# Kernel tuning notes

Measured on AMD Instinct MI355X. Metric: run time of the kernel, lower is better.

## Reference

```python
import jax, jax.numpy as jnp
import numpy as np

N0, N1, N2 = 200000, 100000, 50000
E0, E1 = 1600000, 800000
D_IN, H, C, K = 256, 256, 7, 40  # in_feats, n_hidden, center_num, n_classes


def setup_inputs() -> dict:
    key = jax.random.key(0)
    ks = jax.random.split(key, 11)
    s = 0.05
    inputs = jax.random.normal(ks[0], (N0, D_IN), jnp.float32)
    edge_src0 = jax.random.randint(ks[1], (E0,), 0, N0, jnp.int32)
    edge_dst0 = jax.random.randint(ks[2], (E0,), 0, N1, jnp.int32)
    edge_src1 = jax.random.randint(ks[3], (E1,), 0, N1, jnp.int32)
    edge_dst1 = jax.random.randint(ks[4], (E1,), 0, N2, jnp.int32)
    W_self0 = jax.random.normal(ks[5], (H, D_IN), jnp.float32) * s
    W_neigh0 = jax.random.normal(ks[6], (H, D_IN), jnp.float32) * s
    b0 = jnp.zeros((H,), jnp.float32)
    W_self1 = jax.random.normal(ks[7], (H, H), jnp.float32) * s
    W_neigh1 = jax.random.normal(ks[8], (H, H), jnp.float32) * s
    b1 = jnp.zeros((H,), jnp.float32)
    W_prompt = jax.random.normal(ks[9], (C, 2 * H), jnp.float32) * s
    W_pp = jax.random.normal(ks[10], (C, K, 2 * H), jnp.float32) * s
    return dict(inputs=inputs, W_self0=W_self0, W_neigh0=W_neigh0, b0=b0,
                W_self1=W_self1, W_neigh1=W_neigh1, b1=b1,
                W_prompt=W_prompt, W_pp=W_pp,
                edge_src0=edge_src0, edge_dst0=edge_dst0,
                edge_src1=edge_src1, edge_dst1=edge_dst1)


def _sage_conv(h_src, h_dst, esrc, edst, n_dst, W_self, W_neigh, b):
    # DGL SAGEConv('mean'): fc_self(h_dst) + fc_neigh(mean_{u in N(v)} h_src[u]) + bias
    msg = h_src[esrc]                                            # [E, d]
    summ = jax.ops.segment_sum(msg, edst, num_segments=n_dst)    # [n_dst, d]
    deg = jax.ops.segment_sum(jnp.ones((esrc.shape[0],), msg.dtype), edst,
                              num_segments=n_dst)                # [n_dst]
    mean = summ / jnp.maximum(deg, 1.0)[:, None]
    return h_dst @ W_self.T + mean @ W_neigh.T + b


def _forward(inputs, W_self0, W_neigh0, b0, W_self1, W_neigh1, b1,
             W_prompt, W_pp, edge_src0, edge_dst0, edge_src1, edge_dst1):
    h = inputs  # dropout=0.0 (eval): identity
    # layer 0: N0 src -> N1 dst
    h_dst = h[:N1]
    h = _sage_conv(h, h_dst, edge_src0, edge_dst0, N1, W_self0, W_neigh0, b0)
    h = jax.nn.relu(h)
    # layer 1: N1 src -> N2 dst
    h_dst = h[:N2]
    h = _sage_conv(h, h_dst, edge_src1, edge_dst1, N2, W_self1, W_neigh1, b1)
    h = jax.nn.relu(h)
    neighbor = jax.nn.relu(h_dst)
    hcat = jnp.concatenate([h, neighbor], axis=1)                # [N2, 2H]
    scores = hcat @ W_prompt.T                                   # [N2, C]
    index = jnp.argmax(scores, axis=1)                           # [N2]
    # per-cluster expert Linear, top-1 dispatch/combine
    all_out = jnp.einsum('nd,ckd->nck', hcat, W_pp)              # [N2, C, K]
    out = jnp.take_along_axis(all_out, index[:, None, None], axis=1)[:, 0, :]
    return out


def reference(inputs, W_self0, W_neigh0, b0, W_self1, W_neigh1, b1,
              W_prompt, W_pp, edge_src0, edge_dst0, edge_src1, edge_dst1):
    return _forward(inputs, W_self0, W_neigh0, b0, W_self1, W_neigh1, b1,
                    W_prompt, W_pp, edge_src0, edge_dst0, edge_src1, edge_dst1)
```

## Files before the change

### kernel.cpp

```cpp
#include <hip/hip_runtime.h>
#include <stdint.h>

typedef unsigned short u16;
typedef unsigned int   u32;
typedef float f32x4  __attribute__((ext_vector_type(4)));
typedef _Float16 f16x4 __attribute__((ext_vector_type(4)));
typedef _Float16 f16x8 __attribute__((ext_vector_type(8)));

#define NN0 200000
#define NN1 100000
#define NN2 50000
#define EE0 1600000
#define EE1 800000
#define DD  256
#define CC  7
#define KK  40

#define LVL2_U16 4096
#define IMG_U16  8192

static __device__ __forceinline__ void split2(float x, _Float16& t0, _Float16& t1) {
    t0 = (_Float16)x;
    t1 = (_Float16)(x - (float)t0);
}

static __device__ __forceinline__ f16x8 pack8(const _Float16* h) {
    f16x8 v;
#pragma unroll
    for (int i = 0; i < 8; ++i) v[i] = h[i];
    return v;
}

static __device__ __forceinline__ void async16(const void* g, void* l) {
    __builtin_amdgcn_global_load_lds(
        (const __attribute__((address_space(1))) void*)g,
        (__attribute__((address_space(3))) void*)l, 16, 0, 0);
}

__global__ void hist_kernel(const int* __restrict__ dst, int* __restrict__ cnt, int n) {
    int i = blockIdx.x * blockDim.x + threadIdx.x;
    if (i < n) atomicAdd(&cnt[dst[i]], 1);
}

__global__ void scan_block_kernel(const int* __restrict__ in, int* __restrict__ out,
                                  int* __restrict__ partials, int n) {
    __shared__ int sd[256];
    int t = threadIdx.x;
    int base = blockIdx.x * 1024 + t * 4;
    int v0 = (base + 0 < n) ? in[base + 0] : 0;
    int v1 = (base + 1 < n) ? in[base + 1] : 0;
    int v2 = (base + 2 < n) ? in[base + 2] : 0;
    int v3 = (base + 3 < n) ? in[base + 3] : 0;
    int p0 = v0, p1 = p0 + v1, p2 = p1 + v2, p3 = p2 + v3;
    sd[t] = p3;
    __syncthreads();
    for (int off = 1; off < 256; off <<= 1) {
        int x = (t >= off) ? sd[t - off] : 0;
        __syncthreads();
        sd[t] += x;
        __syncthreads();
    }
    int excl = sd[t] - p3;
    if (base + 0 < n) out[base + 0] = excl + p0;
    if (base + 1 < n) out[base + 1] = excl + p1;
    if (base + 2 < n) out[base + 2] = excl + p2;
    if (base + 3 < n) out[base + 3] = excl + p3;
    if (t == 255) partials[blockIdx.x] = sd[255];
}

__global__ void scan_partials_kernel(int* __restrict__ partials, int nb) {
    __shared__ int sd[256];
    int t = threadIdx.x;
    int v = (t < nb) ? partials[t] : 0;
    sd[t] = v;
    __syncthreads();
    for (int off = 1; off < 256; off <<= 1) {
        int x = (t >= off) ? sd[t - off] : 0;
        __syncthreads();
        sd[t] += x;
        __syncthreads();
    }
    if (t < nb) partials[t] = sd[t];
}

__global__ void scan_add_kernel(int* __restrict__ out, const int* __restrict__ partials, int n) {
    int b = blockIdx.x;
    if (b == 0) return;
    int add = partials[b - 1];
    int base = b * 1024 + threadIdx.x * 4;
    if (base + 0 < n) out[base + 0] += add;
    if (base + 1 < n) out[base + 1] += add;
    if (base + 2 < n) out[base + 2] += add;
    if (base + 3 < n) out[base + 3] += add;
}

__global__ void fill_kernel(const int* __restrict__ esrc, const int* __restrict__ edst,
                            const int* __restrict__ rp, int* __restrict__ cur,
                            int* __restrict__ ss, int n) {
    int i = blockIdx.x * blockDim.x + threadIdx.x;
    if (i < n) {
        int d = edst[i];
        int p = rp[d] + atomicAdd(&cur[d], 1);
        ss[p] = esrc[i];
    }
}

__global__ void to_fp16(const float* __restrict__ in, _Float16* __restrict__ outp, long n) {
    long i = ((long)blockIdx.x * blockDim.x + threadIdx.x) * 8;
    if (i >= n) return;
    f32x4 a = *reinterpret_cast<const f32x4*>(in + i);
    f32x4 b = *reinterpret_cast<const f32x4*>(in + i + 4);
    f16x8 h;
    h[0] = (_Float16)a[0]; h[1] = (_Float16)a[1]; h[2] = (_Float16)a[2]; h[3] = (_Float16)a[3];
    h[4] = (_Float16)b[0]; h[5] = (_Float16)b[1]; h[6] = (_Float16)b[2]; h[7] = (_Float16)b[3];
    *reinterpret_cast<f16x8*>(outp + i) = h;
}

__global__ void gather_mean_fp16(const _Float16* __restrict__ Xh, const int* __restrict__ rp,
                                 const int* __restrict__ ss, float* __restrict__ mean, int ndst) {
    int wave = threadIdx.x >> 6, lane = threadIdx.x & 63;
    int d = blockIdx.x * 4 + wave;
    if (d >= ndst) return;
    int beg = rp[d], end = rp[d + 1];
    int lo4 = lane * 4;
    f32x4 a0 = (f32x4)(0.f), a1 = (f32x4)(0.f), a2 = (f32x4)(0.f), a3 = (f32x4)(0.f);
    int j = beg;
    for (; j + 8 <= end; j += 8) {
        int s0 = ss[j + 0], s1 = ss[j + 1], s2 = ss[j + 2], s3 = ss[j + 3];
        int s4 = ss[j + 4], s5 = ss[j + 5], s6 = ss[j + 6], s7 = ss[j + 7];
        f16x4 h0 = *reinterpret_cast<const f16x4*>(Xh + (size_t)s0 * DD + lo4);
        f16x4 h1 = *reinterpret_cast<const f16x4*>(Xh + (size_t)s1 * DD + lo4);
        f16x4 h2 = *reinterpret_cast<const f16x4*>(Xh + (size_t)s2 * DD + lo4);
        f16x4 h3 = *reinterpret_cast<const f16x4*>(Xh + (size_t)s3 * DD + lo4);
        f16x4 h4 = *reinterpret_cast<const f16x4*>(Xh + (size_t)s4 * DD + lo4);
        f16x4 h5 = *reinterpret_cast<const f16x4*>(Xh + (size_t)s5 * DD + lo4);
        f16x4 h6 = *reinterpret_cast<const f16x4*>(Xh + (size_t)s6 * DD + lo4);
        f16x4 h7 = *reinterpret_cast<const f16x4*>(Xh + (size_t)s7 * DD + lo4);
        a0 += __builtin_convertvector(h0, f32x4);
        a1 += __builtin_convertvector(h1, f32x4);
        a2 += __builtin_convertvector(h2, f32x4);
        a3 += __builtin_convertvector(h3, f32x4);
        a0 += __builtin_convertvector(h4, f32x4);
        a1 += __builtin_convertvector(h5, f32x4);
        a2 += __builtin_convertvector(h6, f32x4);
        a3 += __builtin_convertvector(h7, f32x4);
    }
    for (; j + 4 <= end; j += 4) {
        int s0 = ss[j + 0], s1 = ss[j + 1], s2 = ss[j + 2], s3 = ss[j + 3];
        f16x4 h0 = *reinterpret_cast<const f16x4*>(Xh + (size_t)s0 * DD + lo4);
        f16x4 h1 = *reinterpret_cast<const f16x4*>(Xh + (size_t)s1 * DD + lo4);
        f16x4 h2 = *reinterpret_cast<const f16x4*>(Xh + (size_t)s2 * DD + lo4);
        f16x4 h3 = *reinterpret_cast<const f16x4*>(Xh + (size_t)s3 * DD + lo4);
        a0 += __builtin_convertvector(h0, f32x4);
        a1 += __builtin_convertvector(h1, f32x4);
        a2 += __builtin_convertvector(h2, f32x4);
        a3 += __builtin_convertvector(h3, f32x4);
    }
    for (; j < end; ++j) {
        int s = ss[j];
        f16x4 h0 = *reinterpret_cast<const f16x4*>(Xh + (size_t)s * DD + lo4);
        a0 += __builtin_convertvector(h0, f32x4);
    }
    f32x4 s = (a0 + a1) + (a2 + a3);
    int dg = end - beg;
    float inv = 1.0f / (float)(dg > 0 ? dg : 1);
    s *= inv;
    *reinterpret_cast<f32x4*>(mean + (size_t)d * DD + lo4) = s;
}

__global__ void build_wimg(const float* __restrict__ Wa0, const float* __restrict__ Wb0,
                           const float* __restrict__ Wa1, const float* __restrict__ Wb1,
                           u16* __restrict__ img) {
    int blk = blockIdx.x;
    int layer = blk >> 5;
    int ntile = (blk >> 4) & 1;
    int chunk = blk & 15;
    const float* Wa = layer ? Wa1 : Wa0;
    const float* Wb = layer ? Wb1 : Wb0;
    int t = threadIdx.x;
    int row = t >> 1, half = t & 1;
    int n = ntile * 128 + row;
    int kg = chunk * 32 + half * 16;
    const float* W = (kg < 256) ? Wa : Wb;
    int kk = kg & 255;
    const float* src = W + (size_t)n * 256 + kk;
    float x[16];
#pragma unroll
    for (int j = 0; j < 16; j += 4) {
        float4 v = *reinterpret_cast<const float4*>(src + j);
        x[j] = v.x; x[j + 1] = v.y; x[j + 2] = v.z; x[j + 3] = v.w;
    }
    _Float16 h0[16], h1[16];
#pragma unroll
    for (int j = 0; j < 16; ++j) split2(x[j], h0[j], h1[j]);
    int rs = (row >> 1) & 3;
    int q0 = (half * 2 + 0) ^ rs;
    int q1 = (half * 2 + 1) ^ rs;
    u16* base = img + (size_t)blk * IMG_U16 + row * 32;
    *reinterpret_cast<f16x8*>(base + q0 * 8)            = pack8(h0);
    *reinterpret_cast<f16x8*>(base + q1 * 8)            = pack8(h0 + 8);
    *reinterpret_cast<f16x8*>(base + LVL2_U16 + q0 * 8) = pack8(h1);
    *reinterpret_cast<f16x8*>(base + LVL2_U16 + q1 * 8) = pack8(h1 + 8);
}

__global__ __launch_bounds__(256, 3) void gemm_f16(const float* __restrict__ X0,
                                                   const float* __restrict__ X1,
                                                   const u16* __restrict__ imgL,
                                                   const float* __restrict__ bias,
                                                   float* __restrict__ out,
                                                   _Float16* __restrict__ outh, int M) {
    __shared__ __align__(16) u16 Asl[2 * LVL2_U16];
    __shared__ __align__(16) u16 Bsl[2 * LVL2_U16];
    int t = threadIdx.x;
    int wave = t >> 6, lane = t & 63;
    int m0 = blockIdx.x * 128;
    int ntile = blockIdx.y;
    int wy = wave >> 1, wx = wave & 1;

    f32x4 acc[4][4];
#pragma unroll
    for (int i = 0; i < 4; ++i)
#pragma unroll
        for (int j = 0; j < 4; ++j) acc[i][j] = (f32x4)(0.f);

    int arow_l = t >> 1;
    int akh = t & 1;
    int arow = m0 + arow_l; if (arow >= M) arow = M - 1;

    int fr = lane & 15;
    int q  = lane >> 4;
    int frm = wy * 64 + fr;
    int frn = wx * 64 + fr;

    const u16* imgT = imgL + (size_t)ntile * 16 * IMG_U16;

    for (int c = 0; c < 16; ++c) {
        const char* src = (const char*)(imgT + (size_t)c * IMG_U16);
#pragma unroll
        for (int i = 0; i < 4; ++i) {
            int seg = wave * 4 + i;
            async16(src + seg * 1024 + lane * 16, (char*)Bsl + seg * 1024 + lane * 16);
        }
        {
            const float* Xs = (c < 8) ? X0 : X1;
            int kc = (c & 7) * 32;
            const float* p = Xs + (size_t)arow * 256 + kc + akh * 16;
            float x[16];
#pragma unroll
            for (int j = 0; j < 16; j += 4) {
                float4 v = *reinterpret_cast<const float4*>(p + j);
                x[j] = v.x; x[j + 1] = v.y; x[j + 2] = v.z; x[j + 3] = v.w;
            }
            _Float16 h0[16], h1[16];
#pragma unroll
            for (int j = 0; j < 16; ++j) split2(x[j], h0[j], h1[j]);
            int rs = (arow_l >> 1) & 3;
            int q0 = (akh * 2 + 0) ^ rs;
            int q1 = (akh * 2 + 1) ^ rs;
            u16* d = Asl + arow_l * 32;
            *reinterpret_cast<f16x8*>(d + q0 * 8)            = pack8(h0);
            *reinterpret_cast<f16x8*>(d + q1 * 8)            = pack8(h0 + 8);
            *reinterpret_cast<f16x8*>(d + LVL2_U16 + q0 * 8) = pack8(h1);
            *reinterpret_cast<f16x8*>(d + LVL2_U16 + q1 * 8) = pack8(h1 + 8);
        }
        __syncthreads();
        f16x8 bf[4][2];
#pragma unroll
        for (int ns = 0; ns < 4; ++ns) {
            int r = frn + ns * 16;
            int off = r * 32 + ((q ^ ((r >> 1) & 3))) * 8;
            bf[ns][0] = *reinterpret_cast<const f16x8*>(Bsl + off);
            bf[ns][1] = *reinterpret_cast<const f16x8*>(Bsl + LVL2_U16 + off);
        }
#pragma unroll
        for (int ms = 0; ms < 4; ++ms) {
            int r = frm + ms * 16;
            int off = r * 32 + ((q ^ ((r >> 1) & 3))) * 8;
            f16x8 af0 = *reinterpret_cast<const f16x8*>(Asl + off);
            f16x8 af1 = *reinterpret_cast<const f16x8*>(Asl + LVL2_U16 + off);
#pragma unroll
            for (int ns = 0; ns < 4; ++ns) {
                f32x4 a = acc[ms][ns];
                a = __builtin_amdgcn_mfma_f32_16x16x32_f16(af0, bf[ns][0], a, 0, 0, 0);
                a = __builtin_amdgcn_mfma_f32_16x16x32_f16(af0, bf[ns][1], a, 0, 0, 0);
                a = __builtin_amdgcn_mfma_f32_16x16x32_f16(af1, bf[ns][0], a, 0, 0, 0);
                acc[ms][ns] = a;
            }
        }
        __syncthreads();
    }
#pragma unroll
    for (int ms = 0; ms < 4; ++ms) {
        int rbase = m0 + wy * 64 + ms * 16 + (lane >> 4) * 4;
#pragma unroll
        for (int ns = 0; ns < 4; ++ns) {
            int col = ntile * 128 + wx * 64 + ns * 16 + (lane & 15);
            float bcol = bias[col];
#pragma unroll
            for (int r = 0; r < 4; ++r) {
                int row = rbase + r;
                if (row < M) {
                    float v = fmaxf(acc[ms][ns][r] + bcol, 0.f);
                    out[(size_t)row * DD + col] = v;
                    if (outh) outh[(size_t)row * DD + col] = (_Float16)v;
                }
            }
        }
    }
}

__global__ void final_kernel(const float* __restrict__ h2, const float* __restrict__ h1,
                             const float* __restrict__ Wp, const float* __restrict__ Wpp,
                             float* __restrict__ out) {
    int wave = threadIdx.x >> 6, lane = threadIdx.x & 63;
    int nd = blockIdx.x * 4 + wave;
    if (nd >= NN2) return;
    int d0 = lane * 8;
    const float* src = (d0 < 256) ? (h2 + (size_t)nd * DD + d0)
                                  : (h1 + (size_t)nd * DD + (d0 - 256));
    float4 v0 = *reinterpret_cast<const float4*>(src);
    float4 v1 = *reinterpret_cast<const float4*>(src + 4);
    float x[8] = {v0.x, v0.y, v0.z, v0.w, v1.x, v1.y, v1.z, v1.w};

    float best = -3.0e38f; int bc = 0;
#pragma unroll
    for (int c = 0; c < CC; ++c) {
        const float* w = Wp + (size_t)c * 512 + d0;
        float4 w0 = *reinterpret_cast<const float4*>(w);
        float4 w1 = *reinterpret_cast<const float4*>(w + 4);
        float p = x[0] * w0.x + x[1] * w0.y + x[2] * w0.z + x[3] * w0.w
                + x[4] * w1.x + x[5] * w1.y + x[6] * w1.z + x[7] * w1.w;
        p += __shfl_xor(p, 32); p += __shfl_xor(p, 16); p += __shfl_xor(p, 8);
        p += __shfl_xor(p, 4);  p += __shfl_xor(p, 2);  p += __shfl_xor(p, 1);
        if (p > best) { best = p; bc = c; }
    }
    for (int k = 0; k < KK; ++k) {
        const float* w = Wpp + ((size_t)bc * KK + k) * 512 + d0;
        float4 w0 = *reinterpret_cast<const float4*>(w);
        float4 w1 = *reinterpret_cast<const float4*>(w + 4);
        float p = x[0] * w0.x + x[1] * w0.y + x[2] * w0.z + x[3] * w0.w
                + x[4] * w1.x + x[5] * w1.y + x[6] * w1.z + x[7] * w1.w;
        p += __shfl_xor(p, 32); p += __shfl_xor(p, 16); p += __shfl_xor(p, 8);
        p += __shfl_xor(p, 4);  p += __shfl_xor(p, 2);  p += __shfl_xor(p, 1);
        if (lane == 0) out[(size_t)nd * KK + k] = p;
    }
}

extern "C" void kernel_launch(void* const* d_in, const int* in_sizes, int n_in,
                              void* d_out, int out_size, void* d_ws, size_t ws_size,
                              hipStream_t stream) {
    const float* inputs  = (const float*)d_in[0];
    const float* Wself0  = (const float*)d_in[1];
    const float* Wneigh0 = (const float*)d_in[2];
    const float* b0      = (const float*)d_in[3];
    const float* Wself1  = (const float*)d_in[4];
    const float* Wneigh1 = (const float*)d_in[5];
    const float* b1      = (const float*)d_in[6];
    const float* Wp      = (const float*)d_in[7];
    const float* Wpp     = (const float*)d_in[8];
    const int* es0 = (const int*)d_in[9];
    const int* ed0 = (const int*)d_in[10];
    const int* es1 = (const int*)d_in[11];
    const int* ed1 = (const int*)d_in[12];

    char* ws = (char*)d_ws;
    size_t off = 0;
    auto alloc = [&](size_t bytes) -> void* {
        void* p = (void*)(ws + off);
        off += (bytes + 255) & ~(size_t)255;
        return p;
    };
    int* cnt0 = (int*)alloc((size_t)NN1 * 4);
    int* cnt1 = (int*)alloc((size_t)NN2 * 4);
    int* cur0 = (int*)alloc((size_t)NN1 * 4);
    int* cur1 = (int*)alloc((size_t)NN2 * 4);
    int* rp0  = (int*)alloc((size_t)(NN1 + 1) * 4);
    int* rp1  = (int*)alloc((size_t)(NN2 + 1) * 4);
    int* part0 = (int*)alloc(1024);
    int* part1 = (int*)alloc(1024);
    size_t zero_bytes = off;
    int*   ss0   = (int*)alloc((size_t)EE0 * 4);
    int*   ss1   = (int*)alloc((size_t)EE1 * 4);
    u16*   wimg  = (u16*)alloc((size_t)64 * IMG_U16 * 2);
    _Float16* xh = (_Float16*)alloc((size_t)NN0 * DD * 2);
    float*    h1 = (float*)xh;
    _Float16* h1h  = (_Float16*)alloc((size_t)NN1 * DD * 2);
    float* mean0 = (float*)alloc((size_t)NN1 * DD * 4);
    float* mean1 = mean0;
    float* h2    = mean0 + (size_t)NN2 * DD;

    hipMemsetAsync(d_ws, 0, zero_bytes, stream);

    hist_kernel<<<(EE0 + 255) / 256, 256, 0, stream>>>(ed0, cnt0, EE0);
    hist_kernel<<<(EE1 + 255) / 256, 256, 0, stream>>>(ed1, cnt1, EE1);
    int nb0 = (NN1 + 1023) / 1024, nb1 = (NN2 + 1023) / 1024;
    scan_block_kernel<<<nb0, 256, 0, stream>>>(cnt0, rp0 + 1, part0, NN1);
    scan_partials_kernel<<<1, 256, 0, stream>>>(part0, nb0);
    scan_add_kernel<<<nb0, 256, 0, stream>>>(rp0 + 1, part0, NN1);
    scan_block_kernel<<<nb1, 256, 0, stream>>>(cnt1, rp1 + 1, part1, NN2);
    scan_partials_kernel<<<1, 256, 0, stream>>>(part1, nb1);
    scan_add_kernel<<<nb1, 256, 0, stream>>>(rp1 + 1, part1, NN2);
    fill_kernel<<<(EE0 + 255) / 256, 256, 0, stream>>>(es0, ed0, rp0, cur0, ss0, EE0);
    fill_kernel<<<(EE1 + 255) / 256, 256, 0, stream>>>(es1, ed1, rp1, cur1, ss1, EE1);

    build_wimg<<<64, 256, 0, stream>>>(Wself0, Wneigh0, Wself1, Wneigh1, wimg);

    long nx = (long)NN0 * DD;
    to_fp16<<<(int)(nx / 8 / 256), 256, 0, stream>>>(inputs, xh, nx);

    gather_mean_fp16<<<(NN1 + 3) / 4, 256, 0, stream>>>(xh, rp0, ss0, mean0, NN1);
    dim3 g0((NN1 + 127) / 128, 2);
    gemm_f16<<<g0, 256, 0, stream>>>(inputs, mean0, wimg, b0, h1, h1h, NN1);

    gather_mean_fp16<<<(NN2 + 3) / 4, 256, 0, stream>>>(h1h, rp1, ss1, mean1, NN2);
    dim3 g1((NN2 + 127) / 128, 2);
    gemm_f16<<<g1, 256, 0, stream>>>(h1, mean1, wimg + (size_t)32 * IMG_U16, b1, h2, nullptr, NN2);

    final_kernel<<<(NN2 + 3) / 4, 256, 0, stream>>>(h2, h1, Wp, Wpp, (float*)d_out);
}
```

Measured before the change: 1.114 ms.

## Split final head into scoring, per-cluster bucketing, and grouped expert projection

The fused final kernel is replaced by four kernels. One computes argmax cluster scores with 16 lanes per node, the next two build counts and a node list grouped by cluster, and the last computes the expert projection over nodes sorted by cluster. Sorting nodes by cluster lets neighbouring waves share the same expert weights in cache, and narrower 16-lane reductions cut the number of shuffles. The cost is three extra launches and an extra pass that re-reads the node features.

```diff
diff --git a/kernel.cpp b/kernel.cpp
--- a/kernel.cpp
+++ b/kernel.cpp
@@ -309,40 +309,99 @@
     }
 }
 
-__global__ void final_kernel(const float* __restrict__ h2, const float* __restrict__ h1,
-                             const float* __restrict__ Wp, const float* __restrict__ Wpp,
-                             float* __restrict__ out) {
-    int wave = threadIdx.x >> 6, lane = threadIdx.x & 63;
-    int nd = blockIdx.x * 4 + wave;
-    if (nd >= NN2) return;
-    int d0 = lane * 8;
-    const float* src = (d0 < 256) ? (h2 + (size_t)nd * DD + d0)
-                                  : (h1 + (size_t)nd * DD + (d0 - 256));
-    float4 v0 = *reinterpret_cast<const float4*>(src);
-    float4 v1 = *reinterpret_cast<const float4*>(src + 4);
-    float x[8] = {v0.x, v0.y, v0.z, v0.w, v1.x, v1.y, v1.z, v1.w};
-
+__global__ void score_kernel(const float* __restrict__ h2, const float* __restrict__ h1,
+                             const float* __restrict__ Wp, int* __restrict__ bcout,
+                             int* __restrict__ gcnt) {
+    __shared__ int lcnt[CC];
+    int t = threadIdx.x;
+    if (t < CC) lcnt[t] = 0;
+    __syncthreads();
+    int wave = t >> 6, lane = t & 63;
+    int ns = lane >> 4, g = lane & 15;
+    int n = (blockIdx.x * 4 + wave) * 4 + ns;
+    int d0 = g * 32;
+    const float* src = (d0 < 256) ? (h2 + (size_t)n * DD + d0)
+                                  : (h1 + (size_t)n * DD + (d0 - 256));
+    f32x4 x[8];
+#pragma unroll
+    for (int j = 0; j < 8; ++j) x[j] = *reinterpret_cast<const f32x4*>(src + j * 4);
     float best = -3.0e38f; int bc = 0;
 #pragma unroll
     for (int c = 0; c < CC; ++c) {
         const float* w = Wp + (size_t)c * 512 + d0;
-        float4 w0 = *reinterpret_cast<const float4*>(w);
-        float4 w1 = *reinterpret_cast<const float4*>(w + 4);
-        float p = x[0] * w0.x + x[1] * w0.y + x[2] * w0.z + x[3] * w0.w
-                + x[4] * w1.x + x[5] * w1.y + x[6] * w1.z + x[7] * w1.w;
-        p += __shfl_xor(p, 32); p += __shfl_xor(p, 16); p += __shfl_xor(p, 8);
-        p += __shfl_xor(p, 4);  p += __shfl_xor(p, 2);  p += __shfl_xor(p, 1);
+        f32x4 a = (f32x4)(0.f);
+#pragma unroll
+        for (int j = 0; j < 8; ++j)
+            a += x[j] * *reinterpret_cast<const f32x4*>(w + j * 4);
+        float p = (a[0] + a[1]) + (a[2] + a[3]);
+        p += __shfl_xor(p, 1, 16);
+        p += __shfl_xor(p, 2, 16);
+        p += __shfl_xor(p, 4, 16);
+        p += __shfl_xor(p, 8, 16);
         if (p > best) { best = p; bc = c; }
     }
+    if (g == 0) {
+        bcout[n] = bc;
+        atomicAdd(&lcnt[bc], 1);
+    }
+    __syncthreads();
+    if (t < CC) atomicAdd(&gcnt[t], lcnt[t]);
+}
+
+__global__ void scan7_kernel(const int* __restrict__ gcnt, int* __restrict__ cbase,
+                             int* __restrict__ cur7) {
+    if (threadIdx.x == 0 && blockIdx.x == 0) {
+        int s = 0;
+        for (int c = 0; c < CC; ++c) { cbase[c] = s; s += gcnt[c]; cur7[c] = 0; }
+        cbase[CC] = s;
+    }
+}
+
+__global__ void fillc_kernel(const int* __restrict__ bc, const int* __restrict__ cbase,
+                             int* __restrict__ cur7, int* __restrict__ nlist) {
+    __shared__ int lcnt[CC];
+    __shared__ int lbase[CC];
+    int t = threadIdx.x;
+    int n = blockIdx.x * 256 + t;
+    if (t < CC) lcnt[t] = 0;
+    __syncthreads();
+    int c = 0, myofs = 0;
+    bool act = n < NN2;
+    if (act) { c = bc[n]; myofs = atomicAdd(&lcnt[c], 1); }
+    __syncthreads();
+    if (t < CC) lbase[t] = lcnt[t] ? atomicAdd(&cur7[t], lcnt[t]) : 0;
+    __syncthreads();
+    if (act) nlist[cbase[c] + lbase[c] + myofs] = n;
+}
+
+__global__ void proj_kernel(const float* __restrict__ h2, const float* __restrict__ h1,
+                            const float* __restrict__ Wpp, const int* __restrict__ nlist,
+                            const int* __restrict__ bcin, float* __restrict__ out) {
+    int t = threadIdx.x;
+    int wave = t >> 6, lane = t & 63;
+    int ns = lane >> 4, g = lane & 15;
+    int i = (blockIdx.x * 4 + wave) * 4 + ns;
+    int n = nlist[i];
+    int c = bcin[n];
+    int d0 = g * 32;
+    const float* src = (d0 < 256) ? (h2 + (size_t)n * DD + d0)
+                                  : (h1 + (size_t)n * DD + (d0 - 256));
+    f32x4 x[8];
+#pragma unroll
+    for (int j = 0; j < 8; ++j) x[j] = *reinterpret_cast<const f32x4*>(src + j * 4);
+    const float* wb = Wpp + (size_t)c * KK * 512 + d0;
     for (int k = 0; k < KK; ++k) {
-        const float* w = Wpp + ((size_t)bc * KK + k) * 512 + d0;
-        float4 w0 = *reinterpret_cast<const float4*>(w);
-        float4 w1 = *reinterpret_cast<const float4*>(w + 4);
-        float p = x[0] * w0.x + x[1] * w0.y + x[2] * w0.z + x[3] * w0.w
-                + x[4] * w1.x + x[5] * w1.y + x[6] * w1.z + x[7] * w1.w;
-        p += __shfl_xor(p, 32); p += __shfl_xor(p, 16); p += __shfl_xor(p, 8);
-        p += __shfl_xor(p, 4);  p += __shfl_xor(p, 2);  p += __shfl_xor(p, 1);
-        if (lane == 0) out[(size_t)nd * KK + k] = p;
+        const float* w = wb + (size_t)k * 512;
+        f32x4 a = (f32x4)(0.f);
+#pragma unroll
+        for (int j = 0; j < 8; ++j)
+            a += x[j] * *reinterpret_cast<const f32x4*>(w + j * 4);
+        float p = (a[0] + a[1]) + (a[2] + a[3]);
+        p += __shfl_xor(p, 1, 16);
+        p += __shfl_xor(p, 2, 16);
+        p += __shfl_xor(p, 4, 16);
+        p += __shfl_xor(p, 8, 16);
+        if (g == (k & 15)) out[(size_t)n * KK + k] = p;
     }
 }
 
@@ -378,9 +437,14 @@
     int* rp1  = (int*)alloc((size_t)(NN2 + 1) * 4);
     int* part0 = (int*)alloc(1024);
     int* part1 = (int*)alloc(1024);
+    int* gcnt  = (int*)alloc(CC * 4);
     size_t zero_bytes = off;
     int*   ss0   = (int*)alloc((size_t)EE0 * 4);
     int*   ss1   = (int*)alloc((size_t)EE1 * 4);
+    int*   bc    = (int*)alloc((size_t)NN2 * 4);
+    int*   nlist = (int*)alloc((size_t)NN2 * 4);
+    int*   cbase = (int*)alloc((CC + 1) * 4);
+    int*   cur7  = (int*)alloc(CC * 4);
     u16*   wimg  = (u16*)alloc((size_t)64 * IMG_U16 * 2);
     _Float16* xh = (_Float16*)alloc((size_t)NN0 * DD * 2);
     float*    h1 = (float*)xh;
@@ -416,5 +480,8 @@
     dim3 g1((NN2 + 127) / 128, 2);
     gemm_f16<<<g1, 256, 0, stream>>>(h1, mean1, wimg + (size_t)32 * IMG_U16, b1, h2, nullptr, NN2);
 
-    final_kernel<<<(NN2 + 3) / 4, 256, 0, stream>>>(h2, h1, Wp, Wpp, (float*)d_out);
-}
+    score_kernel<<<NN2 / 16, 256, 0, stream>>>(h2, h1, Wp, bc, gcnt);
+    scan7_kernel<<<1, 64, 0, stream>>>(gcnt, cbase, cur7);
+    fillc_kernel<<<(NN2 + 255) / 256, 256, 0, stream>>>(bc, cbase, cur7, nlist);
+    proj_kernel<<<NN2 / 16, 256, 0, stream>>>(h2, h1, Wpp, nlist, bc, (float*)d_out);
+}
```

Result: slower. 1.511 ms (+35.6%).

## Compute prompt scores and all expert outputs with MFMA GEMM, then select

Applied to the files above, without the earlier changes.

Replaces the per-node wave-reduction head kernel with a dense fp16-split MFMA GEMM over all 7 prompt rows and all 280 expert rows (padded to 288 columns), followed by a small kernel that takes the argmax and copies the chosen 40 outputs. It targets the shuffle-reduction and scalar-FMA cost of the old head, which ran dot products serially with many cross-lane reductions. In exchange it computes every expert's outputs instead of only the selected one and adds a 50000x288 fp32 intermediate buffer. The argmax now uses split-fp16 MFMA results, so near-ties could pick a different expert than before.

```diff
diff --git a/kernel.cpp b/kernel.cpp
--- a/kernel.cpp
+++ b/kernel.cpp
@@ -15,6 +15,7 @@
 #define DD  256
 #define CC  7
 #define KK  40
+#define NHEAD 288
 
 #define LVL2_U16 4096
 #define IMG_U16  8192
@@ -203,12 +204,49 @@
     *reinterpret_cast<f16x8*>(base + LVL2_U16 + q1 * 8) = pack8(h1 + 8);
 }
 
+__global__ void build_wimg_head(const float* __restrict__ Wp, const float* __restrict__ Wpp,
+                                u16* __restrict__ img) {
+    int blk = blockIdx.x;
+    int ntile = blk >> 4;
+    int chunk = blk & 15;
+    int t = threadIdx.x;
+    int row = t >> 1, half = t & 1;
+    int r = ntile * 128 + row;
+    int kg = chunk * 32 + half * 16;
+    float x[16];
+    const float* src = nullptr;
+    if (r < CC)            src = Wp  + (size_t)r * 512 + kg;
+    else if (r < CC + CC * KK) src = Wpp + (size_t)(r - CC) * 512 + kg;
+    if (src) {
+#pragma unroll
+        for (int j = 0; j < 16; j += 4) {
+            float4 v = *reinterpret_cast<const float4*>(src + j);
+            x[j] = v.x; x[j + 1] = v.y; x[j + 2] = v.z; x[j + 3] = v.w;
+        }
+    } else {
+#pragma unroll
+        for (int j = 0; j < 16; ++j) x[j] = 0.f;
+    }
+    _Float16 h0[16], h1[16];
+#pragma unroll
+    for (int j = 0; j < 16; ++j) split2(x[j], h0[j], h1[j]);
+    int rs = (row >> 1) & 3;
+    int q0 = (half * 2 + 0) ^ rs;
+    int q1 = (half * 2 + 1) ^ rs;
+    u16* base = img + (size_t)blk * IMG_U16 + row * 32;
+    *reinterpret_cast<f16x8*>(base + q0 * 8)            = pack8(h0);
+    *reinterpret_cast<f16x8*>(base + q1 * 8)            = pack8(h0 + 8);
+    *reinterpret_cast<f16x8*>(base + LVL2_U16 + q0 * 8) = pack8(h1);
+    *reinterpret_cast<f16x8*>(base + LVL2_U16 + q1 * 8) = pack8(h1 + 8);
+}
+
 __global__ __launch_bounds__(256, 3) void gemm_f16(const float* __restrict__ X0,
                                                    const float* __restrict__ X1,
                                                    const u16* __restrict__ imgL,
                                                    const float* __restrict__ bias,
                                                    float* __restrict__ out,
-                                                   _Float16* __restrict__ outh, int M) {
+                                                   _Float16* __restrict__ outh,
+                                                   int M, int ldo, int dorelu) {
     __shared__ __align__(16) u16 Asl[2 * LVL2_U16];
     __shared__ __align__(16) u16 Bsl[2 * LVL2_U16];
     int t = threadIdx.x;
@@ -295,13 +333,15 @@
 #pragma unroll
         for (int ns = 0; ns < 4; ++ns) {
             int col = ntile * 128 + wx * 64 + ns * 16 + (lane & 15);
-            float bcol = bias[col];
+            if (col >= ldo) continue;
+            float bcol = bias ? bias[col] : 0.f;
 #pragma unroll
             for (int r = 0; r < 4; ++r) {
                 int row = rbase + r;
                 if (row < M) {
-                    float v = fmaxf(acc[ms][ns][r] + bcol, 0.f);
-                    out[(size_t)row * DD + col] = v;
+                    float v = acc[ms][ns][r] + bcol;
+                    if (dorelu) v = fmaxf(v, 0.f);
+                    out[(size_t)row * ldo + col] = v;
                     if (outh) outh[(size_t)row * DD + col] = (_Float16)v;
                 }
             }
@@ -309,41 +349,18 @@
     }
 }
 
-__global__ void final_kernel(const float* __restrict__ h2, const float* __restrict__ h1,
-                             const float* __restrict__ Wp, const float* __restrict__ Wpp,
-                             float* __restrict__ out) {
+__global__ void select_kernel(const float* __restrict__ all, float* __restrict__ out) {
     int wave = threadIdx.x >> 6, lane = threadIdx.x & 63;
-    int nd = blockIdx.x * 4 + wave;
-    if (nd >= NN2) return;
-    int d0 = lane * 8;
-    const float* src = (d0 < 256) ? (h2 + (size_t)nd * DD + d0)
-                                  : (h1 + (size_t)nd * DD + (d0 - 256));
-    float4 v0 = *reinterpret_cast<const float4*>(src);
-    float4 v1 = *reinterpret_cast<const float4*>(src + 4);
-    float x[8] = {v0.x, v0.y, v0.z, v0.w, v1.x, v1.y, v1.z, v1.w};
-
-    float best = -3.0e38f; int bc = 0;
-#pragma unroll
-    for (int c = 0; c < CC; ++c) {
-        const float* w = Wp + (size_t)c * 512 + d0;
-        float4 w0 = *reinterpret_cast<const float4*>(w);
-        float4 w1 = *reinterpret_cast<const float4*>(w + 4);
-        float p = x[0] * w0.x + x[1] * w0.y + x[2] * w0.z + x[3] * w0.w
-                + x[4] * w1.x + x[5] * w1.y + x[6] * w1.z + x[7] * w1.w;
-        p += __shfl_xor(p, 32); p += __shfl_xor(p, 16); p += __shfl_xor(p, 8);
-        p += __shfl_xor(p, 4);  p += __shfl_xor(p, 2);  p += __shfl_xor(p, 1);
-        if (p > best) { best = p; bc = c; }
-    }
-    for (int k = 0; k < KK; ++k) {
-        const float* w = Wpp + ((size_t)bc * KK + k) * 512 + d0;
-        float4 w0 = *reinterpret_cast<const float4*>(w);
-        float4 w1 = *reinterpret_cast<const float4*>(w + 4);
-        float p = x[0] * w0.x + x[1] * w0.y + x[2] * w0.z + x[3] * w0.w
-                + x[4] * w1.x + x[5] * w1.y + x[6] * w1.z + x[7] * w1.w;
-        p += __shfl_xor(p, 32); p += __shfl_xor(p, 16); p += __shfl_xor(p, 8);
-        p += __shfl_xor(p, 4);  p += __shfl_xor(p, 2);  p += __shfl_xor(p, 1);
-        if (lane == 0) out[(size_t)nd * KK + k] = p;
-    }
+    int n = blockIdx.x * 4 + wave;
+    if (n >= NN2) return;
+    const float* row = all + (size_t)n * NHEAD;
+    float best = row[0]; int bc = 0;
+#pragma unroll
+    for (int c = 1; c < CC; ++c) {
+        float s = row[c];
+        if (s > best) { best = s; bc = c; }
+    }
+    if (lane < KK) out[(size_t)n * KK + lane] = row[CC + bc * KK + lane];
 }
 
 extern "C" void kernel_launch(void* const* d_in, const int* in_sizes, int n_in,
@@ -381,13 +398,15 @@
     size_t zero_bytes = off;
     int*   ss0   = (int*)alloc((size_t)EE0 * 4);
     int*   ss1   = (int*)alloc((size_t)EE1 * 4);
-    u16*   wimg  = (u16*)alloc((size_t)64 * IMG_U16 * 2);
+    u16*   wimg  = (u16*)alloc((size_t)(64 + 48) * IMG_U16 * 2);
+    u16*   wimgH = wimg + (size_t)64 * IMG_U16;
     _Float16* xh = (_Float16*)alloc((size_t)NN0 * DD * 2);
     float*    h1 = (float*)xh;
     _Float16* h1h  = (_Float16*)alloc((size_t)NN1 * DD * 2);
     float* mean0 = (float*)alloc((size_t)NN1 * DD * 4);
     float* mean1 = mean0;
     float* h2    = mean0 + (size_t)NN2 * DD;
+    float* allout = (float*)alloc((size_t)NN2 * NHEAD * 4);
 
     hipMemsetAsync(d_ws, 0, zero_bytes, stream);
 
@@ -404,17 +423,20 @@
     fill_kernel<<<(EE1 + 255) / 256, 256, 0, stream>>>(es1, ed1, rp1, cur1, ss1, EE1);
 
     build_wimg<<<64, 256, 0, stream>>>(Wself0, Wneigh0, Wself1, Wneigh1, wimg);
+    build_wimg_head<<<48, 256, 0, stream>>>(Wp, Wpp, wimgH);
 
     long nx = (long)NN0 * DD;
     to_fp16<<<(int)(nx / 8 / 256), 256, 0, stream>>>(inputs, xh, nx);
 
     gather_mean_fp16<<<(NN1 + 3) / 4, 256, 0, stream>>>(xh, rp0, ss0, mean0, NN1);
     dim3 g0((NN1 + 127) / 128, 2);
-    gemm_f16<<<g0, 256, 0, stream>>>(inputs, mean0, wimg, b0, h1, h1h, NN1);
+    gemm_f16<<<g0, 256, 0, stream>>>(inputs, mean0, wimg, b0, h1, h1h, NN1, DD, 1);
 
     gather_mean_fp16<<<(NN2 + 3) / 4, 256, 0, stream>>>(h1h, rp1, ss1, mean1, NN2);
     dim3 g1((NN2 + 127) / 128, 2);
-    gemm_f16<<<g1, 256, 0, stream>>>(h1, mean1, wimg + (size_t)32 * IMG_U16, b1, h2, nullptr, NN2);
-
-    final_kernel<<<(NN2 + 3) / 4, 256, 0, stream>>>(h2, h1, Wp, Wpp, (float*)d_out);
-}
+    gemm_f16<<<g1, 256, 0, stream>>>(h1, mean1, wimg + (size_t)32 * IMG_U16, b1, h2, nullptr, NN2, DD, 1);
+
+    dim3 gh((NN2 + 127) / 128, 3);
+    gemm_f16<<<gh, 256, 0, stream>>>(h2, h1, wimgH, nullptr, allout, nullptr, NN2, NHEAD, 0);
+    select_kernel<<<(NN2 + 3) / 4, 256, 0, stream>>>(allout, (float*)d_out);
+}
```

After: 1.042 ms. -6.5%, faster.
